# Optimization experiments

Hardware: AMD Instinct MI355X
Metric: run time of the kernel (lower is better)

The kernel has to match this reference:

```python
import jax, jax.numpy as jnp
import numpy as np

N = 50000       # nodes
E = 500000      # directed edges
Q_EDGES = 100000
F_IN = 128
HID = 64
K = 2           # Chebyshev order -> K+1 weight slices
LABEL = 2
Q_PHASE = 0.25
TWO_PI = 2.0 * np.pi


def setup_inputs() -> dict:
    key = jax.random.key(0)
    ks = jax.random.split(key, 9)
    real = jax.random.normal(ks[0], (N, F_IN), jnp.float32)
    imag = jax.random.normal(ks[1], (N, F_IN), jnp.float32)
    src = jax.random.randint(ks[2], (E,), 0, N)
    off = jax.random.randint(ks[3], (E,), 1, N)
    dst = (src + off) % N  # no self loops (torch code removes them)
    edge_index = jnp.stack([src, dst]).astype(jnp.int64)
    query_edges = jax.random.randint(ks[4], (Q_EDGES, 2), 0, N).astype(jnp.int64)
    edge_weight = jax.random.uniform(ks[5], (E,), jnp.float32, 0.5, 1.5)
    W1 = jax.random.normal(ks[6], (K + 1, F_IN, HID), jnp.float32) / np.sqrt(F_IN)
    b1 = jnp.zeros((HID,), jnp.float32)
    W2 = jax.random.normal(ks[7], (K + 1, HID, HID), jnp.float32) / np.sqrt(HID)
    b2 = jnp.zeros((HID,), jnp.float32)
    Wlin = jax.random.normal(ks[8], (LABEL, 4 * HID), jnp.float32) / np.sqrt(4 * HID)
    blin = jnp.zeros((LABEL,), jnp.float32)
    return dict(real=real, imag=imag, edge_index=edge_index, query_edges=query_edges,
                edge_weight=edge_weight, W1=W1, b1=b1, W2=W2, b2=b2, Wlin=Wlin, blin=blin)


def magnetic_norm(edge_index, edge_weight, num_nodes, q):
    """Edge weights of scaled magnetic Laplacian L_hat = L - I (sym norm, lambda_max=2).

    Returns symmetrized edge list (2E edges) with real/imag coefficients
    -D^{-1/2} A_s D^{-1/2} * exp(i * theta), theta = 2*pi*q*(A - A^T).
    """
    u, v = edge_index[0], edge_index[1]
    s = jnp.concatenate([u, v])                  # source (j)
    d = jnp.concatenate([v, u])                  # target (i)
    w_sym = jnp.concatenate([edge_weight, edge_weight]) * 0.5  # A_s = (A + A^T)/2
    theta = TWO_PI * q * jnp.concatenate([edge_weight, -edge_weight])
    deg = jax.ops.segment_sum(w_sym, s, num_segments=num_nodes)
    dinv = jnp.where(deg > 0, jax.lax.rsqrt(jnp.where(deg > 0, deg, 1.0)), 0.0)
    norm = dinv[s] * w_sym * dinv[d]
    return s, d, -norm * jnp.cos(theta), -norm * jnp.sin(theta)


def magnet_conv(xr, xi, s, d, nr, ni, W, b, num_nodes):
    def prop(x, c):  # out[i] = sum_{e: d_e = i} c_e * x[s_e]
        return jax.ops.segment_sum(c[:, None] * x[s], d, num_segments=num_nodes)

    xs = (xr, xi, xr, xi)            # streams: real_real, imag_imag, imag_real, real_imag
    cs = (nr, ni, ni, nr)            # norm used by each stream
    T0 = xs
    out = [x @ W[0] for x in T0]
    T1 = tuple(prop(x, c) for x, c in zip(xs, cs))
    out = [o + t @ W[1] for o, t in zip(out, T1)]
    for k in range(2, W.shape[0]):
        T2 = tuple(2.0 * prop(t1, c) - t0 for t0, t1, c in zip(T0, T1, cs))
        out = [o + t @ W[k] for o, t in zip(out, T2)]
        T0, T1 = T1, T2
    out_r = out[0] - out[1] + b
    out_i = out[2] + out[3] + b
    return out_r, out_i


def complex_relu(xr, xi):
    mask = (xr >= 0).astype(xr.dtype)
    return xr * mask, xi * mask


def reference(real, imag, edge_index, query_edges, edge_weight, W1, b1, W2, b2, Wlin, blin):
    num_nodes = real.shape[0]
    s, d, nr, ni = magnetic_norm(edge_index, edge_weight, num_nodes, Q_PHASE)
    xr, xi = magnet_conv(real, imag, s, d, nr, ni, W1, b1, num_nodes)
    xr, xi = complex_relu(xr, xi)
    xr, xi = magnet_conv(xr, xi, s, d, nr, ni, W2, b2, num_nodes)
    xr, xi = complex_relu(xr, xi)
    q0, q1 = query_edges[:, 0], query_edges[:, 1]
    x = jnp.concatenate([xr[q0], xr[q1], xi[q0], xi[q1]], axis=-1)  # [Q, 4*hidden]
    # dropout is identity in eval mode
    logits = x @ Wlin.T + blin
    return jax.nn.log_softmax(logits, axis=1)
```

## Files before the change

kernel.cpp:

```cpp
#include <hip/hip_runtime.h>


__device__ __forceinline__ float4 ld4(const float* __restrict__ p) {
  return *reinterpret_cast<const float4*>(p);
}
__device__ __forceinline__ float2 ld2(const float* __restrict__ p) {
  return *reinterpret_cast<const float2*>(p);
}

template <int K>
__global__ __launch_bounds__(256) void k_gemm_deg(
    const int* __restrict__ u, const int* __restrict__ v,
    const float* __restrict__ w, unsigned long long* __restrict__ dc, int E,
    int epb,
    const float* __restrict__ Ar, const float* __restrict__ Ai,
    const float* __restrict__ W,
    const float* __restrict__ bias,
    float* __restrict__ P1, float* __restrict__ P2,
    float* __restrict__ Hr, float* __restrict__ Hi, int M) {
  __shared__ float Asr[32][36];
  __shared__ float Asi[32][36];
  __shared__ float Ws1[32][64];
  __shared__ float Ws2[32][64];
  __shared__ float Wsm[32][64];
  const int t = threadIdx.x;
  {
    int e0 = blockIdx.x * epb;
    int e1 = min(e0 + epb, E);
    for (int e = e0 + t; e < e1; e += 256) {
      float hw = 0.5f * w[e];
      unsigned fx = __float2uint_rn(hw * 16777216.f);
      unsigned long long pk = (1ULL << 32) | (unsigned long long)fx;
      atomicAdd(&dc[u[e]], pk);
      atomicAdd(&dc[v[e]], pk);
    }
  }
  const int r0 = blockIdx.x * 32;
  const int tc = t & 15, tr = t >> 4;
  const float* W0 = W;
  const float* W1 = W + (size_t)K * 64;
  const float* W2 = W + (size_t)2 * K * 64;
  float a1r[2][4] = {}, a1i[2][4] = {}, a2r[2][4] = {}, a2i[2][4] = {};
  float amr[2][4] = {}, ami[2][4] = {};
  for (int k0 = 0; k0 < K; k0 += 32) {
    {
      int row = t >> 3, c4 = t & 7;
      int gr = r0 + row;
      float4 fr = make_float4(0.f, 0.f, 0.f, 0.f), fi = fr;
      if (gr < M) {
        fr = ld4(&Ar[(size_t)gr * K + k0 + c4 * 4]);
        fi = ld4(&Ai[(size_t)gr * K + k0 + c4 * 4]);
      }
      *reinterpret_cast<float4*>(&Asr[row][c4 * 4]) = fr;
      *reinterpret_cast<float4*>(&Asi[row][c4 * 4]) = fi;
    }
    for (int li = t; li < 512; li += 256) {
      int row = li >> 4, c4 = li & 15;
      size_t woff = (size_t)(k0 + row) * 64 + c4 * 4;
      float4 w1 = ld4(&W1[woff]);
      float4 w2 = ld4(&W2[woff]);
      float4 w0 = ld4(&W0[woff]);
      *reinterpret_cast<float4*>(&Ws1[row][c4 * 4]) = w1;
      *reinterpret_cast<float4*>(&Ws2[row][c4 * 4]) = w2;
      *reinterpret_cast<float4*>(&Wsm[row][c4 * 4]) =
          make_float4(w0.x - w2.x, w0.y - w2.y, w0.z - w2.z, w0.w - w2.w);
    }
    __syncthreads();
#pragma unroll 4
    for (int k = 0; k < 32; ++k) {
      float4 b1 = *reinterpret_cast<const float4*>(&Ws1[k][tc * 4]);
      float4 b2 = *reinterpret_cast<const float4*>(&Ws2[k][tc * 4]);
      float4 bm = *reinterpret_cast<const float4*>(&Wsm[k][tc * 4]);
#pragma unroll
      for (int i = 0; i < 2; ++i) {
        float ar = Asr[tr * 2 + i][k], ai = Asi[tr * 2 + i][k];
        a1r[i][0] += ar * b1.x; a1r[i][1] += ar * b1.y; a1r[i][2] += ar * b1.z; a1r[i][3] += ar * b1.w;
        a1i[i][0] += ai * b1.x; a1i[i][1] += ai * b1.y; a1i[i][2] += ai * b1.z; a1i[i][3] += ai * b1.w;
        a2r[i][0] += ar * b2.x; a2r[i][1] += ar * b2.y; a2r[i][2] += ar * b2.z; a2r[i][3] += ar * b2.w;
        a2i[i][0] += ai * b2.x; a2i[i][1] += ai * b2.y; a2i[i][2] += ai * b2.z; a2i[i][3] += ai * b2.w;
        amr[i][0] += ar * bm.x; amr[i][1] += ar * bm.y; amr[i][2] += ar * bm.z; amr[i][3] += ar * bm.w;
        ami[i][0] += ai * bm.x; ami[i][1] += ai * bm.y; ami[i][2] += ai * bm.z; ami[i][3] += ai * bm.w;
      }
    }
    __syncthreads();
  }
  float b0 = bias[tc * 4 + 0], bb1 = bias[tc * 4 + 1];
  float b2v = bias[tc * 4 + 2], b3 = bias[tc * 4 + 3];
#pragma unroll
  for (int i = 0; i < 2; ++i) {
    int gr = r0 + tr * 2 + i;
    if (gr >= M) continue;
    size_t pb = (size_t)gr * 128 + tc * 8;
    *reinterpret_cast<float4*>(&P1[pb]) =
        make_float4(a1r[i][0], a1i[i][0], a1r[i][1], a1i[i][1]);
    *reinterpret_cast<float4*>(&P1[pb + 4]) =
        make_float4(a1r[i][2], a1i[i][2], a1r[i][3], a1i[i][3]);
    *reinterpret_cast<float4*>(&P2[pb]) =
        make_float4(a2r[i][0], a2i[i][0], a2r[i][1], a2i[i][1]);
    *reinterpret_cast<float4*>(&P2[pb + 4]) =
        make_float4(a2r[i][2], a2i[i][2], a2r[i][3], a2i[i][3]);
    size_t hb = (size_t)gr * 64 + tc * 4;
    *reinterpret_cast<float4*>(&Hr[hb]) =
        make_float4(amr[i][0] - ami[i][0] + b0, amr[i][1] - ami[i][1] + bb1,
                    amr[i][2] - ami[i][2] + b2v, amr[i][3] - ami[i][3] + b3);
    *reinterpret_cast<float4*>(&Hi[hb]) =
        make_float4(amr[i][0] + ami[i][0] + b0, amr[i][1] + ami[i][1] + bb1,
                    amr[i][2] + ami[i][2] + b2v, amr[i][3] + ami[i][3] + b3);
  }
}

template <int K>
__global__ __launch_bounds__(256) void k_gemmF(
    const float* __restrict__ Ar, const float* __restrict__ Ai,
    const float* __restrict__ W, const float* __restrict__ bias,
    float* __restrict__ P1, float* __restrict__ P2,
    float* __restrict__ Hr, float* __restrict__ Hi, int M) {
  __shared__ float Asr[32][36];
  __shared__ float Asi[32][36];
  __shared__ float Ws1[32][64];
  __shared__ float Ws2[32][64];
  __shared__ float Wsm[32][64];
  const int t = threadIdx.x;
  const int r0 = blockIdx.x * 32;
  const int tc = t & 15, tr = t >> 4;
  const float* W0 = W;
  const float* W1 = W + (size_t)K * 64;
  const float* W2 = W + (size_t)2 * K * 64;
  float a1r[2][4] = {}, a1i[2][4] = {}, a2r[2][4] = {}, a2i[2][4] = {};
  float amr[2][4] = {}, ami[2][4] = {};
  for (int k0 = 0; k0 < K; k0 += 32) {
    {
      int row = t >> 3, c4 = t & 7;
      int gr = r0 + row;
      float4 fr = make_float4(0.f, 0.f, 0.f, 0.f), fi = fr;
      if (gr < M) {
        fr = ld4(&Ar[(size_t)gr * K + k0 + c4 * 4]);
        fi = ld4(&Ai[(size_t)gr * K + k0 + c4 * 4]);
      }
      *reinterpret_cast<float4*>(&Asr[row][c4 * 4]) = fr;
      *reinterpret_cast<float4*>(&Asi[row][c4 * 4]) = fi;
    }
    for (int li = t; li < 512; li += 256) {
      int row = li >> 4, c4 = li & 15;
      size_t woff = (size_t)(k0 + row) * 64 + c4 * 4;
      float4 w1 = ld4(&W1[woff]);
      float4 w2 = ld4(&W2[woff]);
      float4 w0 = ld4(&W0[woff]);
      *reinterpret_cast<float4*>(&Ws1[row][c4 * 4]) = w1;
      *reinterpret_cast<float4*>(&Ws2[row][c4 * 4]) = w2;
      *reinterpret_cast<float4*>(&Wsm[row][c4 * 4]) =
          make_float4(w0.x - w2.x, w0.y - w2.y, w0.z - w2.z, w0.w - w2.w);
    }
    __syncthreads();
#pragma unroll 4
    for (int k = 0; k < 32; ++k) {
      float4 b1 = *reinterpret_cast<const float4*>(&Ws1[k][tc * 4]);
      float4 b2 = *reinterpret_cast<const float4*>(&Ws2[k][tc * 4]);
      float4 bm = *reinterpret_cast<const float4*>(&Wsm[k][tc * 4]);
#pragma unroll
      for (int i = 0; i < 2; ++i) {
        float ar = Asr[tr * 2 + i][k], ai = Asi[tr * 2 + i][k];
        a1r[i][0] += ar * b1.x; a1r[i][1] += ar * b1.y; a1r[i][2] += ar * b1.z; a1r[i][3] += ar * b1.w;
        a1i[i][0] += ai * b1.x; a1i[i][1] += ai * b1.y; a1i[i][2] += ai * b1.z; a1i[i][3] += ai * b1.w;
        a2r[i][0] += ar * b2.x; a2r[i][1] += ar * b2.y; a2r[i][2] += ar * b2.z; a2r[i][3] += ar * b2.w;
        a2i[i][0] += ai * b2.x; a2i[i][1] += ai * b2.y; a2i[i][2] += ai * b2.z; a2i[i][3] += ai * b2.w;
        amr[i][0] += ar * bm.x; amr[i][1] += ar * bm.y; amr[i][2] += ar * bm.z; amr[i][3] += ar * bm.w;
        ami[i][0] += ai * bm.x; ami[i][1] += ai * bm.y; ami[i][2] += ai * bm.z; ami[i][3] += ai * bm.w;
      }
    }
    __syncthreads();
  }
  float b0 = bias[tc * 4 + 0], bb1 = bias[tc * 4 + 1];
  float b2v = bias[tc * 4 + 2], b3 = bias[tc * 4 + 3];
#pragma unroll
  for (int i = 0; i < 2; ++i) {
    int gr = r0 + tr * 2 + i;
    if (gr >= M) continue;
    size_t pb = (size_t)gr * 128 + tc * 8;
    *reinterpret_cast<float4*>(&P1[pb]) =
        make_float4(a1r[i][0], a1i[i][0], a1r[i][1], a1i[i][1]);
    *reinterpret_cast<float4*>(&P1[pb + 4]) =
        make_float4(a1r[i][2], a1i[i][2], a1r[i][3], a1i[i][3]);
    *reinterpret_cast<float4*>(&P2[pb]) =
        make_float4(a2r[i][0], a2i[i][0], a2r[i][1], a2i[i][1]);
    *reinterpret_cast<float4*>(&P2[pb + 4]) =
        make_float4(a2r[i][2], a2i[i][2], a2r[i][3], a2i[i][3]);
    size_t hb = (size_t)gr * 64 + tc * 4;
    *reinterpret_cast<float4*>(&Hr[hb]) =
        make_float4(amr[i][0] - ami[i][0] + b0, amr[i][1] - ami[i][1] + bb1,
                    amr[i][2] - ami[i][2] + b2v, amr[i][3] - ami[i][3] + b3);
    *reinterpret_cast<float4*>(&Hi[hb]) =
        make_float4(amr[i][0] + ami[i][0] + b0, amr[i][1] + ami[i][1] + bb1,
                    amr[i][2] + ami[i][2] + b2v, amr[i][3] + ami[i][3] + b3);
  }
}

__global__ __launch_bounds__(256) void k_scan1(
    const unsigned long long* __restrict__ dc, int* __restrict__ rp,
    int* __restrict__ bsum, int N) {
  __shared__ int sh[256];
  int t = threadIdx.x;
  int base = blockIdx.x * 1024 + t * 4;
  int c0 = (base + 0 < N) ? (int)(dc[base + 0] >> 32) : 0;
  int c1 = (base + 1 < N) ? (int)(dc[base + 1] >> 32) : 0;
  int c2 = (base + 2 < N) ? (int)(dc[base + 2] >> 32) : 0;
  int c3 = (base + 3 < N) ? (int)(dc[base + 3] >> 32) : 0;
  int s = c0 + c1 + c2 + c3;
  sh[t] = s;
  __syncthreads();
  for (int o = 1; o < 256; o <<= 1) {
    int y = (t >= o) ? sh[t - o] : 0;
    __syncthreads();
    if (t >= o) sh[t] += y;
    __syncthreads();
  }
  int excl = sh[t] - s;
  if (base + 0 < N) rp[base + 0] = excl;
  if (base + 1 < N) rp[base + 1] = excl + c0;
  if (base + 2 < N) rp[base + 2] = excl + c0 + c1;
  if (base + 3 < N) rp[base + 3] = excl + c0 + c1 + c2;
  if (t == 255) bsum[blockIdx.x] = sh[255];
}

__global__ void k_scan3(int* __restrict__ rp, int* __restrict__ nxt,
                        const int* __restrict__ bsum, int N, int twoE) {
  int i = blockIdx.x * 256 + threadIdx.x;
  if (i > N) return;
  if (i == N) { rp[N] = twoE; return; }
  int b = i >> 10;
  int pre = 0;
  for (int j = 0; j < b; ++j) pre += bsum[j];
  int val = rp[i] + pre;
  rp[i] = val;
  nxt[i] = val;
}

__global__ void k_scatter(const int* __restrict__ u, const int* __restrict__ v,
                          const float* __restrict__ w,
                          const unsigned long long* __restrict__ dc,
                          int* __restrict__ nxt, int* __restrict__ src,
                          float2* __restrict__ cf, int E) {
  int e = blockIdx.x * 256 + threadIdx.x;
  if (e >= E) return;
  int a = u[e], b = v[e];
  float we = w[e];
  float da = (float)(unsigned)dc[a] * (1.f / 16777216.f);
  float db = (float)(unsigned)dc[b] * (1.f / 16777216.f);
  float ia = da > 0.f ? rsqrtf(da) : 0.f;
  float ib = db > 0.f ? rsqrtf(db) : 0.f;
  float norm = ia * (0.5f * we) * ib;
  float th = 1.57079632679489662f * we;
  float sn, cs;
  sincosf(th, &sn, &cs);
  float cr = -norm * cs, ci = -norm * sn;
  int p1 = atomicAdd(&nxt[b], 1);
  src[p1] = a;
  cf[p1] = make_float2(cr, ci);
  int p2 = atomicAdd(&nxt[a], 1);
  src[p2] = b;
  cf[p2] = make_float2(cr, -ci);
}

__global__ __launch_bounds__(256) void k_gU(
    const int* __restrict__ src, const float2* __restrict__ cf,
    const int* __restrict__ rp, const float* __restrict__ P2,
    const float* __restrict__ P1, float* __restrict__ Z, int N) {
  int d = blockIdx.x * 4 + (threadIdx.x >> 6);
  if (d >= N) return;
  int lane = threadIdx.x & 63;
  int g = lane >> 5, lg = lane & 31;
  float4 a01 = {0, 0, 0, 0};
  float4 a23 = {0, 0, 0, 0};
  int k1 = rp[d + 1];
#pragma unroll 2
  for (int k = rp[d] + g; k < k1; k += 2) {
    int s = src[k];
    float2 c = cf[k];
    float4 v = ld4(P2 + (size_t)s * 128 + lg * 4);
    a01.x += c.x * v.x; a01.y += c.y * v.y;
    a01.z += c.x * v.z; a01.w += c.y * v.w;
    a23.x += c.y * v.x; a23.y += c.x * v.y;
    a23.z += c.y * v.z; a23.w += c.x * v.w;
  }
  a01.x += __shfl_xor(a01.x, 32); a01.y += __shfl_xor(a01.y, 32);
  a01.z += __shfl_xor(a01.z, 32); a01.w += __shfl_xor(a01.w, 32);
  a23.x += __shfl_xor(a23.x, 32); a23.y += __shfl_xor(a23.y, 32);
  a23.z += __shfl_xor(a23.z, 32); a23.w += __shfl_xor(a23.w, 32);
  float4 p = ld4(P1 + (size_t)d * 128 + lg * 4);
  size_t zb = (size_t)d * 256 + lg * 4;
  if (g == 0)
    *reinterpret_cast<float4*>(&Z[zb]) =
        make_float4(p.x + 2.f * a01.x, p.y + 2.f * a01.y,
                    p.z + 2.f * a01.z, p.w + 2.f * a01.w);
  else
    *reinterpret_cast<float4*>(&Z[zb + 128]) =
        make_float4(p.x + 2.f * a23.x, p.y + 2.f * a23.y,
                    p.z + 2.f * a23.z, p.w + 2.f * a23.w);
}

__global__ __launch_bounds__(256) void k_gC(
    const int* __restrict__ src, const float2* __restrict__ cf,
    const int* __restrict__ rp, const float* __restrict__ Z,
    float* __restrict__ Hr, float* __restrict__ Hi, int N) {
  int d = blockIdx.x * 4 + (threadIdx.x >> 6);
  if (d >= N) return;
  int lane = threadIdx.x & 63;
  int g = lane >> 5, lg = lane & 31;
  float2 ahr = {0, 0}, ahi = {0, 0};
  int k1 = rp[d + 1];
#pragma unroll 2
  for (int k = rp[d] + g; k < k1; k += 2) {
    int s = src[k];
    float2 c = cf[k];
    const float* row = Z + (size_t)s * 256 + lg * 4;
    float4 z1 = ld4(row);
    float4 z2 = ld4(row + 128);
    ahr.x += c.x * z1.x - c.y * z1.y;
    ahr.y += c.x * z1.z - c.y * z1.w;
    ahi.x += c.y * z2.x + c.x * z2.y;
    ahi.y += c.y * z2.z + c.x * z2.w;
  }
  ahr.x += __shfl_xor(ahr.x, 32);
  ahr.y += __shfl_xor(ahr.y, 32);
  ahi.x += __shfl_xor(ahi.x, 32);
  ahi.y += __shfl_xor(ahi.y, 32);
  if (g == 0) {
    size_t hb = (size_t)d * 64 + lg * 2;
    float2 hr = ld2(&Hr[hb]);
    float2 hi = ld2(&Hi[hb]);
    hr.x += ahr.x; hr.y += ahr.y;
    hi.x += ahi.x; hi.y += ahi.y;
    if (hr.x < 0.f) { hr.x = 0.f; hi.x = 0.f; }
    if (hr.y < 0.f) { hr.y = 0.f; hi.y = 0.f; }
    *reinterpret_cast<float2*>(&Hr[hb]) = hr;
    *reinterpret_cast<float2*>(&Hi[hb]) = hi;
  }
}

__global__ __launch_bounds__(256) void k_query(
    const int* __restrict__ qe, const float* __restrict__ xr,
    const float* __restrict__ xi, const float* __restrict__ Wlin,
    const float* __restrict__ blin, float* __restrict__ out, int Q) {
  int q = blockIdx.x * 4 + (threadIdx.x >> 6);
  if (q >= Q) return;
  int lane = threadIdx.x & 63;
  int q0 = qe[2 * q], q1 = qe[2 * q + 1];
  float x0 = xr[(size_t)q0 * 64 + lane];
  float x1 = xr[(size_t)q1 * 64 + lane];
  float x2 = xi[(size_t)q0 * 64 + lane];
  float x3 = xi[(size_t)q1 * 64 + lane];
  float l0 = x0 * Wlin[lane] + x1 * Wlin[64 + lane] + x2 * Wlin[128 + lane] + x3 * Wlin[192 + lane];
  float l1 = x0 * Wlin[256 + lane] + x1 * Wlin[320 + lane] + x2 * Wlin[384 + lane] + x3 * Wlin[448 + lane];
#pragma unroll
  for (int o = 32; o > 0; o >>= 1) {
    l0 += __shfl_xor(l0, o);
    l1 += __shfl_xor(l1, o);
  }
  if (lane == 0) {
    l0 += blin[0];
    l1 += blin[1];
    float m = fmaxf(l0, l1);
    float lse = m + logf(expf(l0 - m) + expf(l1 - m));
    out[2 * q + 0] = l0 - lse;
    out[2 * q + 1] = l1 - lse;
  }
}

extern "C" void kernel_launch(void* const* d_in, const int* in_sizes, int n_in,
                              void* d_out, int out_size, void* d_ws, size_t ws_size,
                              hipStream_t stream) {
  const float* real = (const float*)d_in[0];
  const float* imag = (const float*)d_in[1];
  const int* ei     = (const int*)d_in[2];
  const int* qe     = (const int*)d_in[3];
  const float* ew   = (const float*)d_in[4];
  const float* W1   = (const float*)d_in[5];
  const float* b1   = (const float*)d_in[6];
  const float* W2   = (const float*)d_in[7];
  const float* b2   = (const float*)d_in[8];
  const float* Wlin = (const float*)d_in[9];
  const float* blin = (const float*)d_in[10];

  const int N = in_sizes[0] / 128;
  const int E = in_sizes[4];
  const int Q = in_sizes[3] / 2;
  const int* u = ei;
  const int* v = ei + E;

  float* ws = (float*)d_ws;
  size_t off = 0;
  auto alloc = [&](size_t n) { float* p = ws + off; off += n; return p; };
  const size_t N64 = (size_t)N * 64;
  const size_t N128 = (size_t)N * 128;
  const size_t N256 = (size_t)N * 256;

  float2* cf = (float2*)alloc((size_t)2 * E * 2);
  unsigned long long* dc = (unsigned long long*)alloc((size_t)2 * N);
  int* src  = (int*)alloc((size_t)2 * E);
  float* P1  = alloc(N128);
  float* P2  = alloc(N128);
  float* Z   = alloc(N256);
  float* HAr = alloc(N64);
  float* HAi = alloc(N64);
  float* HBr = alloc(N64);
  float* HBi = alloc(N64);
  int* rp   = (int*)alloc(N + 1);
  int* nxt  = (int*)alloc(N);
  int* bsum = (int*)alloc(64);
  (void)ws_size; (void)n_in; (void)out_size;

  const int eb = (E + 255) / 256;
  const int mb = (N + 31) / 32;
  const int NB = (N + 1023) / 1024;
  const int gb = (N + 3) / 4;
  const int epb = (E + mb - 1) / mb;

  hipMemsetAsync(dc, 0, (size_t)N * 8, stream);
  k_gemm_deg<128><<<mb, 256, 0, stream>>>(
      u, v, ew, dc, E, epb, real, imag, W1, b1, P1, P2, HAr, HAi, N);
  k_scan1<<<NB, 256, 0, stream>>>(dc, rp, bsum, N);
  k_scan3<<<(N + 256) / 256, 256, 0, stream>>>(rp, nxt, bsum, N, 2 * E);
  k_scatter<<<eb, 256, 0, stream>>>(u, v, ew, dc, nxt, src, cf, E);

  k_gU<<<gb, 256, 0, stream>>>(src, cf, rp, P2, P1, Z, N);
  k_gC<<<gb, 256, 0, stream>>>(src, cf, rp, Z, HAr, HAi, N);

  k_gemmF<64><<<mb, 256, 0, stream>>>(HAr, HAi, W2, b2, P1, P2, HBr, HBi, N);
  k_gU<<<gb, 256, 0, stream>>>(src, cf, rp, P2, P1, Z, N);
  k_gC<<<gb, 256, 0, stream>>>(src, cf, rp, Z, HBr, HBi, N);

  k_query<<<(Q + 3) / 4, 256, 0, stream>>>(qe, HBr, HBi, Wlin, blin, (float*)d_out, Q);
}
```

Measured before the change: 672.0 us.

## Bucket CSR edges by source-range chunk and gather multiple destinations per wave chunk-major

Builds the CSR with each destination's edges split into 16 buckets by source-node range. Each wave now owns 4 (gU) or 8 (gC) destinations and walks bucket by bucket across them, so gathers running at the same moment hit a narrower band of source rows and reuse cache better. Degree accumulation moves from packed 64-bit fixed-point atomics to float atomics plus per-bucket integer counters. In exchange the scan runs over 16x more entries, edge counting needs more atomics, and the many short bucket loops leave fewer waves running and more lanes idle.

Measured after the change: 864.7 us. +28.7%, slower.

```diff
diff --git a/kernel.cpp b/kernel.cpp
--- a/kernel.cpp
+++ b/kernel.cpp
@@ -1,5 +1,7 @@
 #include <hip/hip_runtime.h>
 
+
+#define CHK 16
 
 __device__ __forceinline__ float4 ld4(const float* __restrict__ p) {
   return *reinterpret_cast<const float4*>(p);
@@ -11,11 +13,10 @@
 template <int K>
 __global__ __launch_bounds__(256) void k_gemm_deg(
     const int* __restrict__ u, const int* __restrict__ v,
-    const float* __restrict__ w, unsigned long long* __restrict__ dc, int E,
-    int epb,
+    const float* __restrict__ w, float* __restrict__ deg,
+    int* __restrict__ cnt2, int E, int epb, int N,
     const float* __restrict__ Ar, const float* __restrict__ Ai,
-    const float* __restrict__ W,
-    const float* __restrict__ bias,
+    const float* __restrict__ W, const float* __restrict__ bias,
     float* __restrict__ P1, float* __restrict__ P2,
     float* __restrict__ Hr, float* __restrict__ Hi, int M) {
   __shared__ float Asr[32][36];
@@ -28,11 +29,13 @@
     int e0 = blockIdx.x * epb;
     int e1 = min(e0 + epb, E);
     for (int e = e0 + t; e < e1; e += 256) {
+      int a = u[e], b = v[e];
       float hw = 0.5f * w[e];
-      unsigned fx = __float2uint_rn(hw * 16777216.f);
-      unsigned long long pk = (1ULL << 32) | (unsigned long long)fx;
-      atomicAdd(&dc[u[e]], pk);
-      atomicAdd(&dc[v[e]], pk);
+      unsafeAtomicAdd(&deg[a], hw);
+      unsafeAtomicAdd(&deg[b], hw);
+      int ca = (a * CHK) / N, cb = (b * CHK) / N;
+      atomicAdd(&cnt2[b * CHK + ca], 1);
+      atomicAdd(&cnt2[a * CHK + cb], 1);
     }
   }
   const int r0 = blockIdx.x * 32;
@@ -196,15 +199,15 @@
 }
 
 __global__ __launch_bounds__(256) void k_scan1(
-    const unsigned long long* __restrict__ dc, int* __restrict__ rp,
-    int* __restrict__ bsum, int N) {
+    const int* __restrict__ cnt2, int* __restrict__ rp2,
+    int* __restrict__ bsum, int NC) {
   __shared__ int sh[256];
   int t = threadIdx.x;
   int base = blockIdx.x * 1024 + t * 4;
-  int c0 = (base + 0 < N) ? (int)(dc[base + 0] >> 32) : 0;
-  int c1 = (base + 1 < N) ? (int)(dc[base + 1] >> 32) : 0;
-  int c2 = (base + 2 < N) ? (int)(dc[base + 2] >> 32) : 0;
-  int c3 = (base + 3 < N) ? (int)(dc[base + 3] >> 32) : 0;
+  int c0 = (base + 0 < NC) ? cnt2[base + 0] : 0;
+  int c1 = (base + 1 < NC) ? cnt2[base + 1] : 0;
+  int c2 = (base + 2 < NC) ? cnt2[base + 2] : 0;
+  int c3 = (base + 3 < NC) ? cnt2[base + 3] : 0;
   int s = c0 + c1 + c2 + c3;
   sh[t] = s;
   __syncthreads();
@@ -215,37 +218,36 @@
     __syncthreads();
   }
   int excl = sh[t] - s;
-  if (base + 0 < N) rp[base + 0] = excl;
-  if (base + 1 < N) rp[base + 1] = excl + c0;
-  if (base + 2 < N) rp[base + 2] = excl + c0 + c1;
-  if (base + 3 < N) rp[base + 3] = excl + c0 + c1 + c2;
+  if (base + 0 < NC) rp2[base + 0] = excl;
+  if (base + 1 < NC) rp2[base + 1] = excl + c0;
+  if (base + 2 < NC) rp2[base + 2] = excl + c0 + c1;
+  if (base + 3 < NC) rp2[base + 3] = excl + c0 + c1 + c2;
   if (t == 255) bsum[blockIdx.x] = sh[255];
 }
 
-__global__ void k_scan3(int* __restrict__ rp, int* __restrict__ nxt,
-                        const int* __restrict__ bsum, int N, int twoE) {
+__global__ void k_scan3(int* __restrict__ rp2, int* __restrict__ nxt2,
+                        const int* __restrict__ bsum, int NC, int twoE) {
   int i = blockIdx.x * 256 + threadIdx.x;
-  if (i > N) return;
-  if (i == N) { rp[N] = twoE; return; }
+  if (i > NC) return;
+  if (i == NC) { rp2[NC] = twoE; return; }
   int b = i >> 10;
   int pre = 0;
   for (int j = 0; j < b; ++j) pre += bsum[j];
-  int val = rp[i] + pre;
-  rp[i] = val;
-  nxt[i] = val;
+  int val = rp2[i] + pre;
+  rp2[i] = val;
+  nxt2[i] = val;
 }
 
 __global__ void k_scatter(const int* __restrict__ u, const int* __restrict__ v,
                           const float* __restrict__ w,
-                          const unsigned long long* __restrict__ dc,
-                          int* __restrict__ nxt, int* __restrict__ src,
-                          float2* __restrict__ cf, int E) {
+                          const float* __restrict__ deg,
+                          int* __restrict__ nxt2, int* __restrict__ src,
+                          float2* __restrict__ cf, int E, int N) {
   int e = blockIdx.x * 256 + threadIdx.x;
   if (e >= E) return;
   int a = u[e], b = v[e];
   float we = w[e];
-  float da = (float)(unsigned)dc[a] * (1.f / 16777216.f);
-  float db = (float)(unsigned)dc[b] * (1.f / 16777216.f);
+  float da = deg[a], db = deg[b];
   float ia = da > 0.f ? rsqrtf(da) : 0.f;
   float ib = db > 0.f ? rsqrtf(db) : 0.f;
   float norm = ia * (0.5f * we) * ib;
@@ -253,87 +255,111 @@
   float sn, cs;
   sincosf(th, &sn, &cs);
   float cr = -norm * cs, ci = -norm * sn;
-  int p1 = atomicAdd(&nxt[b], 1);
+  int ca = (a * CHK) / N, cb = (b * CHK) / N;
+  int p1 = atomicAdd(&nxt2[b * CHK + ca], 1);
   src[p1] = a;
   cf[p1] = make_float2(cr, ci);
-  int p2 = atomicAdd(&nxt[a], 1);
+  int p2 = atomicAdd(&nxt2[a * CHK + cb], 1);
   src[p2] = b;
   cf[p2] = make_float2(cr, -ci);
 }
 
 __global__ __launch_bounds__(256) void k_gU(
     const int* __restrict__ src, const float2* __restrict__ cf,
-    const int* __restrict__ rp, const float* __restrict__ P2,
+    const int* __restrict__ rp2, const float* __restrict__ P2,
     const float* __restrict__ P1, float* __restrict__ Z, int N) {
-  int d = blockIdx.x * 4 + (threadIdx.x >> 6);
-  if (d >= N) return;
+  int wave = threadIdx.x >> 6;
+  int d0 = (blockIdx.x * 4 + wave) * 4;
   int lane = threadIdx.x & 63;
   int g = lane >> 5, lg = lane & 31;
-  float4 a01 = {0, 0, 0, 0};
-  float4 a23 = {0, 0, 0, 0};
-  int k1 = rp[d + 1];
-#pragma unroll 2
-  for (int k = rp[d] + g; k < k1; k += 2) {
-    int s = src[k];
-    float2 c = cf[k];
-    float4 v = ld4(P2 + (size_t)s * 128 + lg * 4);
-    a01.x += c.x * v.x; a01.y += c.y * v.y;
-    a01.z += c.x * v.z; a01.w += c.y * v.w;
-    a23.x += c.y * v.x; a23.y += c.x * v.y;
-    a23.z += c.y * v.z; a23.w += c.x * v.w;
-  }
-  a01.x += __shfl_xor(a01.x, 32); a01.y += __shfl_xor(a01.y, 32);
-  a01.z += __shfl_xor(a01.z, 32); a01.w += __shfl_xor(a01.w, 32);
-  a23.x += __shfl_xor(a23.x, 32); a23.y += __shfl_xor(a23.y, 32);
-  a23.z += __shfl_xor(a23.z, 32); a23.w += __shfl_xor(a23.w, 32);
-  float4 p = ld4(P1 + (size_t)d * 128 + lg * 4);
-  size_t zb = (size_t)d * 256 + lg * 4;
-  if (g == 0)
-    *reinterpret_cast<float4*>(&Z[zb]) =
-        make_float4(p.x + 2.f * a01.x, p.y + 2.f * a01.y,
-                    p.z + 2.f * a01.z, p.w + 2.f * a01.w);
-  else
-    *reinterpret_cast<float4*>(&Z[zb + 128]) =
-        make_float4(p.x + 2.f * a23.x, p.y + 2.f * a23.y,
-                    p.z + 2.f * a23.z, p.w + 2.f * a23.w);
+  float4 a01[4] = {}, a23[4] = {};
+  for (int c = 0; c < CHK; ++c) {
+#pragma unroll
+    for (int j = 0; j < 4; ++j) {
+      int d = d0 + j;
+      if (d >= N) continue;
+      int base = d * CHK + c;
+      int k0 = rp2[base], k1 = rp2[base + 1];
+      for (int k = k0 + g; k < k1; k += 2) {
+        int s = src[k];
+        float2 cc = cf[k];
+        float4 vv = ld4(P2 + (size_t)s * 128 + lg * 4);
+        a01[j].x += cc.x * vv.x; a01[j].y += cc.y * vv.y;
+        a01[j].z += cc.x * vv.z; a01[j].w += cc.y * vv.w;
+        a23[j].x += cc.y * vv.x; a23[j].y += cc.x * vv.y;
+        a23[j].z += cc.y * vv.z; a23[j].w += cc.x * vv.w;
+      }
+    }
+  }
+#pragma unroll
+  for (int j = 0; j < 4; ++j) {
+    int d = d0 + j;
+    if (d >= N) continue;
+    a01[j].x += __shfl_xor(a01[j].x, 32); a01[j].y += __shfl_xor(a01[j].y, 32);
+    a01[j].z += __shfl_xor(a01[j].z, 32); a01[j].w += __shfl_xor(a01[j].w, 32);
+    a23[j].x += __shfl_xor(a23[j].x, 32); a23[j].y += __shfl_xor(a23[j].y, 32);
+    a23[j].z += __shfl_xor(a23[j].z, 32); a23[j].w += __shfl_xor(a23[j].w, 32);
+    float4 p = ld4(P1 + (size_t)d * 128 + lg * 4);
+    size_t zb = (size_t)d * 256 + lg * 4;
+    if (g == 0)
+      *reinterpret_cast<float4*>(&Z[zb]) =
+          make_float4(p.x + 2.f * a01[j].x, p.y + 2.f * a01[j].y,
+                      p.z + 2.f * a01[j].z, p.w + 2.f * a01[j].w);
+    else
+      *reinterpret_cast<float4*>(&Z[zb + 128]) =
+          make_float4(p.x + 2.f * a23[j].x, p.y + 2.f * a23[j].y,
+                      p.z + 2.f * a23[j].z, p.w + 2.f * a23[j].w);
+  }
 }
 
 __global__ __launch_bounds__(256) void k_gC(
     const int* __restrict__ src, const float2* __restrict__ cf,
-    const int* __restrict__ rp, const float* __restrict__ Z,
+    const int* __restrict__ rp2, const float* __restrict__ Z,
     float* __restrict__ Hr, float* __restrict__ Hi, int N) {
-  int d = blockIdx.x * 4 + (threadIdx.x >> 6);
-  if (d >= N) return;
+  int wave = threadIdx.x >> 6;
+  int d0 = (blockIdx.x * 4 + wave) * 8;
   int lane = threadIdx.x & 63;
   int g = lane >> 5, lg = lane & 31;
-  float2 ahr = {0, 0}, ahi = {0, 0};
-  int k1 = rp[d + 1];
-#pragma unroll 2
-  for (int k = rp[d] + g; k < k1; k += 2) {
-    int s = src[k];
-    float2 c = cf[k];
-    const float* row = Z + (size_t)s * 256 + lg * 4;
-    float4 z1 = ld4(row);
-    float4 z2 = ld4(row + 128);
-    ahr.x += c.x * z1.x - c.y * z1.y;
-    ahr.y += c.x * z1.z - c.y * z1.w;
-    ahi.x += c.y * z2.x + c.x * z2.y;
-    ahi.y += c.y * z2.z + c.x * z2.w;
-  }
-  ahr.x += __shfl_xor(ahr.x, 32);
-  ahr.y += __shfl_xor(ahr.y, 32);
-  ahi.x += __shfl_xor(ahi.x, 32);
-  ahi.y += __shfl_xor(ahi.y, 32);
-  if (g == 0) {
-    size_t hb = (size_t)d * 64 + lg * 2;
-    float2 hr = ld2(&Hr[hb]);
-    float2 hi = ld2(&Hi[hb]);
-    hr.x += ahr.x; hr.y += ahr.y;
-    hi.x += ahi.x; hi.y += ahi.y;
-    if (hr.x < 0.f) { hr.x = 0.f; hi.x = 0.f; }
-    if (hr.y < 0.f) { hr.y = 0.f; hi.y = 0.f; }
-    *reinterpret_cast<float2*>(&Hr[hb]) = hr;
-    *reinterpret_cast<float2*>(&Hi[hb]) = hi;
+  float2 ahr[8] = {}, ahi[8] = {};
+  for (int c = 0; c < CHK; ++c) {
+#pragma unroll
+    for (int j = 0; j < 8; ++j) {
+      int d = d0 + j;
+      if (d >= N) continue;
+      int base = d * CHK + c;
+      int k0 = rp2[base], k1 = rp2[base + 1];
+      for (int k = k0 + g; k < k1; k += 2) {
+        int s = src[k];
+        float2 cc = cf[k];
+        const float* row = Z + (size_t)s * 256 + lg * 4;
+        float4 z1 = ld4(row);
+        float4 z2 = ld4(row + 128);
+        ahr[j].x += cc.x * z1.x - cc.y * z1.y;
+        ahr[j].y += cc.x * z1.z - cc.y * z1.w;
+        ahi[j].x += cc.y * z2.x + cc.x * z2.y;
+        ahi[j].y += cc.y * z2.z + cc.x * z2.w;
+      }
+    }
+  }
+#pragma unroll
+  for (int j = 0; j < 8; ++j) {
+    int d = d0 + j;
+    if (d >= N) continue;
+    ahr[j].x += __shfl_xor(ahr[j].x, 32);
+    ahr[j].y += __shfl_xor(ahr[j].y, 32);
+    ahi[j].x += __shfl_xor(ahi[j].x, 32);
+    ahi[j].y += __shfl_xor(ahi[j].y, 32);
+    if (g == 0) {
+      size_t hb = (size_t)d * 64 + lg * 2;
+      float2 hr = ld2(&Hr[hb]);
+      float2 hi = ld2(&Hi[hb]);
+      hr.x += ahr[j].x; hr.y += ahr[j].y;
+      hi.x += ahi[j].x; hi.y += ahi[j].y;
+      if (hr.x < 0.f) { hr.x = 0.f; hi.x = 0.f; }
+      if (hr.y < 0.f) { hr.y = 0.f; hi.y = 0.f; }
+      *reinterpret_cast<float2*>(&Hr[hb]) = hr;
+      *reinterpret_cast<float2*>(&Hi[hb]) = hi;
+    }
   }
 }
 
@@ -386,6 +412,7 @@
   const int Q = in_sizes[3] / 2;
   const int* u = ei;
   const int* v = ei + E;
+  const int NC = N * CHK;
 
   float* ws = (float*)d_ws;
   size_t off = 0;
@@ -395,7 +422,6 @@
   const size_t N256 = (size_t)N * 256;
 
   float2* cf = (float2*)alloc((size_t)2 * E * 2);
-  unsigned long long* dc = (unsigned long long*)alloc((size_t)2 * N);
   int* src  = (int*)alloc((size_t)2 * E);
   float* P1  = alloc(N128);
   float* P2  = alloc(N128);
@@ -404,30 +430,34 @@
   float* HAi = alloc(N64);
   float* HBr = alloc(N64);
   float* HBi = alloc(N64);
-  int* rp   = (int*)alloc(N + 1);
-  int* nxt  = (int*)alloc(N);
-  int* bsum = (int*)alloc(64);
+  float* deg = alloc(N);
+  int* cnt2 = (int*)alloc(NC);
+  int* rp2  = (int*)alloc(NC + 1);
+  int* nxt2 = (int*)alloc(NC);
+  int* bsum = (int*)alloc(1024);
   (void)ws_size; (void)n_in; (void)out_size;
 
   const int eb = (E + 255) / 256;
   const int mb = (N + 31) / 32;
-  const int NB = (N + 1023) / 1024;
-  const int gb = (N + 3) / 4;
+  const int NB = (NC + 1023) / 1024;
+  const int gbU = (N + 15) / 16;
+  const int gbC = (N + 31) / 32;
   const int epb = (E + mb - 1) / mb;
 
-  hipMemsetAsync(dc, 0, (size_t)N * 8, stream);
+  hipMemsetAsync(deg, 0, (size_t)N * 4, stream);
+  hipMemsetAsync(cnt2, 0, (size_t)NC * 4, stream);
   k_gemm_deg<128><<<mb, 256, 0, stream>>>(
-      u, v, ew, dc, E, epb, real, imag, W1, b1, P1, P2, HAr, HAi, N);
-  k_scan1<<<NB, 256, 0, stream>>>(dc, rp, bsum, N);
-  k_scan3<<<(N + 256) / 256, 256, 0, stream>>>(rp, nxt, bsum, N, 2 * E);
-  k_scatter<<<eb, 256, 0, stream>>>(u, v, ew, dc, nxt, src, cf, E);
-
-  k_gU<<<gb, 256, 0, stream>>>(src, cf, rp, P2, P1, Z, N);
-  k_gC<<<gb, 256, 0, stream>>>(src, cf, rp, Z, HAr, HAi, N);
+      u, v, ew, deg, cnt2, E, epb, N, real, imag, W1, b1, P1, P2, HAr, HAi, N);
+  k_scan1<<<NB, 256, 0, stream>>>(cnt2, rp2, bsum, NC);
+  k_scan3<<<(NC + 256) / 256, 256, 0, stream>>>(rp2, nxt2, bsum, NC, 2 * E);
+  k_scatter<<<eb, 256, 0, stream>>>(u, v, ew, deg, nxt2, src, cf, E, N);
+
+  k_gU<<<gbU, 256, 0, stream>>>(src, cf, rp2, P2, P1, Z, N);
+  k_gC<<<gbC, 256, 0, stream>>>(src, cf, rp2, Z, HAr, HAi, N);
 
   k_gemmF<64><<<mb, 256, 0, stream>>>(HAr, HAi, W2, b2, P1, P2, HBr, HBi, N);
-  k_gU<<<gb, 256, 0, stream>>>(src, cf, rp, P2, P1, Z, N);
-  k_gC<<<gb, 256, 0, stream>>>(src, cf, rp, Z, HBr, HBi, N);
+  k_gU<<<gbU, 256, 0, stream>>>(src, cf, rp2, P2, P1, Z, N);
+  k_gC<<<gbC, 256, 0, stream>>>(src, cf, rp2, Z, HBr, HBi, N);
 
   k_query<<<(Q + 3) / 4, 256, 0, stream>>>(qe, HBr, HBi, Wlin, blin, (float*)d_out, Q);
 }
```
